# Optimization experiments

Measured on AMD Instinct MI355X. Metric: run time of the kernel, lower is better.

Reference implementation:

```python
import jax, jax.numpy as jnp
import numpy as np

B, S, E, H, D = 1, 2048, 1024, 16, 64
LAM_INIT = 0.8  # \u03bbinit from init_kwargs
LN_EPS = 1e-5


def setup_inputs() -> dict:
    key = jax.random.key(0)
    ks = jax.random.split(key, 6)
    w = 0.02  # weight init scale
    return {
        "X": jax.random.normal(ks[0], (B, S, E), dtype=jnp.float32),
        "Wq": jax.random.normal(ks[1], (H, E, 2 * D), dtype=jnp.float32) * w,
        "bq": jnp.zeros((H, 2 * D), dtype=jnp.float32),
        "Wk": jax.random.normal(ks[2], (H, E, 2 * D), dtype=jnp.float32) * w,
        "bk": jnp.zeros((H, 2 * D), dtype=jnp.float32),
        "Wv": jax.random.normal(ks[3], (H, E, D), dtype=jnp.float32) * w,
        "bv": jnp.zeros((H, D), dtype=jnp.float32),
        "Wo": jax.random.normal(ks[4], (H * D, E), dtype=jnp.float32) * w,
        "bo": jnp.zeros((E,), dtype=jnp.float32),
        "gamma": jnp.ones((E,), dtype=jnp.float32),
        "beta": jnp.zeros((E,), dtype=jnp.float32),
        "lam": jnp.float32(0.5),
    }


def reference(X, Wq, bq, Wk, bk, Wv, bv, Wo, bo, gamma, beta, lam):
    # Batched over heads: Q,K -> [B,H,S,2D], V -> [B,H,S,D]
    Q = jnp.einsum("bse,hec->bhsc", X, Wq) + bq[None, :, None, :]
    K = jnp.einsum("bse,hec->bhsc", X, Wk) + bk[None, :, None, :]
    V = jnp.einsum("bse,hed->bhsd", X, Wv) + bv[None, :, None, :]
    d = Wv.shape[-1]
    Q1, Q2 = Q[..., :d], Q[..., d:]
    K1, K2 = K[..., :d], K[..., d:]
    s = 1.0 / jnp.sqrt(jnp.float32(d))
    A1 = jnp.einsum("bhqd,bhkd->bhqk", Q1, K1) * s
    A2 = jnp.einsum("bhqd,bhkd->bhqk", Q2, K2) * s
    P = jax.nn.softmax(A1, axis=-1) - lam * jax.nn.softmax(A2, axis=-1)
    O = jnp.einsum("bhqk,bhkd->bhqd", P, V)  # [B,H,S,D]
    Ocat = jnp.transpose(O, (0, 2, 1, 3)).reshape(O.shape[0], O.shape[2], -1)  # [B,S,H*D]
    Y = Ocat @ Wo + bo
    mu = jnp.mean(Y, axis=-1, keepdims=True)
    var = jnp.var(Y, axis=-1, keepdims=True)
    Yn = (Y - mu) * jax.lax.rsqrt(var + LN_EPS) * gamma + beta
    return Yn * (1.0 - LAM_INIT)
```

## Files before the change

### kernel.cpp

```cpp
#include <hip/hip_runtime.h>

#define S_LEN 2048
#define EDIM  1024
#define HEADS 16
#define DHEAD 64

typedef __attribute__((ext_vector_type(8))) short bf16x8;
typedef __attribute__((ext_vector_type(4))) short short4v;
typedef __attribute__((ext_vector_type(4))) float f32x4;

__device__ inline unsigned short f2bf(float f) {
    unsigned int u = __float_as_uint(f);
    unsigned int r = (u + 0x7FFFu + ((u >> 16) & 1u)) >> 16;
    return (unsigned short)r;
}
__device__ inline float bf2f(unsigned short b) {
    return __uint_as_float(((unsigned int)b) << 16);
}
__device__ inline void load_lds16(const void* g, void* l) {
    __builtin_amdgcn_global_load_lds(
        (const __attribute__((address_space(1))) unsigned int*)g,
        (__attribute__((address_space(3))) unsigned int*)l, 16, 0, 0);
}

__global__ void k_convert_x(const float* __restrict__ x, short* __restrict__ xb, int n4) {
    int i = blockIdx.x * blockDim.x + threadIdx.x;
    if (i >= n4) return;
    f32x4 v = ((const f32x4*)x)[i];
    short4v o;
    o[0] = (short)f2bf(v[0]); o[1] = (short)f2bf(v[1]);
    o[2] = (short)f2bf(v[2]); o[3] = (short)f2bf(v[3]);
    ((short4v*)xb)[i] = o;
}

__global__ void k_transpose_cvt(const float* __restrict__ in, short* __restrict__ out, int R, int C) {
    __shared__ float tile[32][33];
    const int b = blockIdx.z;
    in  += (size_t)b * R * C;
    out += (size_t)b * R * C;
    const int c0 = blockIdx.x * 32, r0 = blockIdx.y * 32;
    #pragma unroll
    for (int yy = 0; yy < 4; ++yy) {
        int r = r0 + threadIdx.y + yy * 8, c = c0 + threadIdx.x;
        tile[threadIdx.y + yy * 8][threadIdx.x] = (r < R && c < C) ? in[(size_t)r * C + c] : 0.f;
    }
    __syncthreads();
    #pragma unroll
    for (int yy = 0; yy < 4; ++yy) {
        int c = c0 + threadIdx.y + yy * 8, r = r0 + threadIdx.x;
        if (c < C && r < R) out[(size_t)c * R + r] = (short)f2bf(tile[threadIdx.x][threadIdx.y + yy * 8]);
    }
}

template<int BM, int BN, int WR, int WC>
__device__ inline void gemm_core(const char* Ag, int ldaB, const char* Bg, int ldbB,
                                 int K, char* sA, char* sB, f32x4* acc) {
    constexpr int NW = WR * WC;
    constexpr int FM = BM / (WR * 16), FN = BN / (WC * 16);
    constexpr int CA = (BM * 128) / (1024 * NW);
    constexpr int CB = (BN * 128) / (1024 * NW);
    const int lane = threadIdx.x & 63, wave = threadIdx.x >> 6;
    const int rl = lane & 15, g = lane >> 4;
    const int wrow = (wave / WC) * (BM / WR);
    const int wcol = (wave % WC) * (BN / WC);
    const int lr = lane >> 3;
    const int lc = ((lane & 7) ^ lr) << 4;

    for (int t = 0; t < K / 64; ++t) {
        __syncthreads();
        #pragma unroll
        for (int i = 0; i < CA; ++i) {
            const int c = i * NW + wave;
            load_lds16(Ag + (size_t)(c * 8 + lr) * ldaB + t * 128 + lc, sA + c * 1024);
        }
        #pragma unroll
        for (int i = 0; i < CB; ++i) {
            const int c = i * NW + wave;
            load_lds16(Bg + (size_t)(c * 8 + lr) * ldbB + t * 128 + lc, sB + c * 1024);
        }
        __syncthreads();
        #pragma unroll
        for (int kk = 0; kk < 2; ++kk) {
            bf16x8 af[FM], bf[FN];
            #pragma unroll
            for (int f = 0; f < FM; ++f) {
                const int r = wrow + f * 16 + rl;
                af[f] = *(const bf16x8*)(sA + r * 128 + (((kk * 4 + g) ^ (r & 7)) << 4));
            }
            #pragma unroll
            for (int j = 0; j < FN; ++j) {
                const int r = wcol + j * 16 + rl;
                bf[j] = *(const bf16x8*)(sB + r * 128 + (((kk * 4 + g) ^ (r & 7)) << 4));
            }
            #pragma unroll
            for (int f = 0; f < FM; ++f)
                #pragma unroll
                for (int j = 0; j < FN; ++j)
                    acc[f * FN + j] = __builtin_amdgcn_mfma_f32_16x16x32_bf16(af[f], bf[j], acc[f * FN + j], 0, 0, 0);
        }
    }
}

__global__ __launch_bounds__(512) void k_gemm_qkv(
        const short* __restrict__ Xb,
        const short* __restrict__ WqT, const short* __restrict__ WkT, const short* __restrict__ WvT,
        const float* __restrict__ bq, const float* __restrict__ bk, const float* __restrict__ bv,
        short* __restrict__ Qh, short* __restrict__ Kh, short* __restrict__ Vt) {
    __shared__ __align__(16) char sA[16384], sB[16384];
    int id = blockIdx.x;
    id = (id & 7) * 80 + (id >> 3);
    const int mbase = (id % 16) * 128;
    const int y = id / 16;

    const short* Bt; const float* bias; int nbase; int which;
    if (y < 16)      { which = 0; Bt = WqT; bias = bq; nbase = y * 128; }
    else if (y < 32) { which = 1; Bt = WkT; bias = bk; nbase = (y - 16) * 128; }
    else             { which = 2; Bt = WvT; bias = bv; nbase = (y - 32) * 128; }

    f32x4 acc[8];
    #pragma unroll
    for (int i = 0; i < 8; ++i) acc[i] = (f32x4){0.f, 0.f, 0.f, 0.f};

    gemm_core<128, 128, 2, 4>((const char*)Xb + (size_t)mbase * 2048, 2048,
                              (const char*)Bt + (size_t)nbase * 2048, 2048,
                              EDIM, sA, sB, acc);

    const int lane = threadIdx.x & 63, wave = threadIdx.x >> 6;
    const int wr = (wave >> 2) * 64, wc = (wave & 3) * 32;
    const int rl = lane & 15, g = lane >> 4;
    const float qscale = 0.125f * 1.44269504088896f;
    #pragma unroll
    for (int i = 0; i < 4; ++i)
        #pragma unroll
        for (int j = 0; j < 2; ++j)
            #pragma unroll
            for (int jj = 0; jj < 4; ++jj) {
                int s = mbase + wr + i * 16 + g * 4 + jj;
                int n = nbase + wc + j * 16 + rl;
                float v = acc[i * 2 + j][jj] + bias[n];
                if (which == 0) v *= qscale;
                short b16 = (short)f2bf(v);
                if (which == 0)      Qh[((size_t)(n >> 7) * S_LEN + s) * 128 + (n & 127)] = b16;
                else if (which == 1) Kh[((size_t)(n >> 7) * S_LEN + s) * 128 + (n & 127)] = b16;
                else                 Vt[(size_t)n * S_LEN + s] = b16;
            }
}

__global__ __launch_bounds__(512, 4) void k_attn(
        const short* __restrict__ Qh, const short* __restrict__ Kh,
        const short* __restrict__ Vt, const float* __restrict__ lam_p,
        short* __restrict__ Ocat) {
    __shared__ __align__(16) char smem[49152];

    const int lane = threadIdx.x & 63, wave = threadIdx.x >> 6;
    const int rl = lane & 15, g = lane >> 4;
    const int qw = wave & 3, kvg = wave >> 2;
    const int h = blockIdx.y;
    const int qbase = blockIdx.x * 64 + qw * 16;
    const int kx = rl & 7;
    const int swz = (rl & 7) << 4;
    const float MFIX = 6.0f;

    char* Kg0 = smem + kvg * 16384;
    char* Pw  = smem + 32768 + wave * 2048;

    const char* Kgb = (const char*)(Kh + (size_t)h * S_LEN * 128);
    const char* Vgb = (const char*)(Vt + (size_t)h * DHEAD * S_LEN);
    const short* Qp = Qh + (size_t)h * S_LEN * 128;

    const int kc0 = qw * 2, kc1 = qw * 2 + 1;
    const int kofs0 = (lane >> 4) * 256 + (((lane & 15) ^ (lane >> 4)) << 4);
    const int kofs1 = (lane >> 4) * 256 + (((lane & 15) ^ ((lane >> 4) + 4)) << 4);

    auto STAGE = [&](int b, int it) {
        const size_t kv0 = (size_t)(kvg * 1024 + it * 32);
        char* kb = Kg0 + b * 8192;
        load_lds16(Kgb + (kv0 + (size_t)kc0 * 4) * 256 + kofs0, kb + kc0 * 1024);
        load_lds16(Kgb + (kv0 + (size_t)kc1 * 4) * 256 + kofs1, kb + kc1 * 1024);
    };

    STAGE(0, 0);

    bf16x8 qf[2][2];
    #pragma unroll
    for (int p = 0; p < 2; ++p)
        #pragma unroll
        for (int kc = 0; kc < 2; ++kc)
            qf[p][kc] = *(const bf16x8*)&Qp[(size_t)(qbase + rl) * 128 + p * 64 + kc * 32 + g * 8];

    bf16x8 ones;
    #pragma unroll
    for (int i = 0; i < 8; ++i) ones[i] = (short)0x3F80;

    f32x4 acc[2][4], accL[2];
    #pragma unroll
    for (int p = 0; p < 2; ++p) {
        #pragma unroll
        for (int t = 0; t < 4; ++t) acc[p][t] = (f32x4){0.f, 0.f, 0.f, 0.f};
        accL[p] = (f32x4){0.f, 0.f, 0.f, 0.f};
    }

    __syncthreads();

    const int NIT = 1024 / 32;
    for (int it = 0; it < NIT; ++it) {
        const int cur = it & 1;
        if (it + 1 < NIT) STAGE(cur ^ 1, it + 1);
        const char* kb = Kg0 + cur * 8192;
        const size_t kv0 = (size_t)(kvg * 1024 + it * 32);

        bf16x8 vf[4];
        #pragma unroll
        for (int t = 0; t < 4; ++t)
            vf[t] = *(const bf16x8*)(Vgb + (size_t)(t * 16 + rl) * 4096 + (kv0 + g * 8) * 2);

        #pragma unroll
        for (int p = 0; p < 2; ++p) {
            f32x4 sc[2];
            #pragma unroll
            for (int t = 0; t < 2; ++t) {
                f32x4 z = (f32x4){0.f, 0.f, 0.f, 0.f};
                #pragma unroll
                for (int kc = 0; kc < 2; ++kc) {
                    bf16x8 kf = *(const bf16x8*)(kb + t * 4096 + rl * 256 + (((p * 8 + kc * 4 + g) ^ kx) << 4));
                    z = __builtin_amdgcn_mfma_f32_16x16x32_bf16(kf, qf[p][kc], z, 0, 0, 0);
                }
                sc[t] = z;
            }

            #pragma unroll
            for (int t = 0; t < 2; ++t) {
                #pragma unroll
                for (int jjp = 0; jjp < 4; jjp += 2) {
                    float e0 = exp2f(sc[t][jjp]     - MFIX);
                    float e1 = exp2f(sc[t][jjp + 1] - MFIX);
                    unsigned u;
                    asm("v_cvt_pk_bf16_f32 %0, %1, %2" : "=v"(u) : "v"(e0), "v"(e1));
                    *(unsigned*)(Pw + rl * 128 + ((p * 64 + (t * 16 + g * 4 + jjp) * 2) ^ swz)) = u;
                }
            }

            bf16x8 pa = *(const bf16x8*)(Pw + rl * 128 + ((p * 64 + g * 16) ^ swz));
            accL[p] = __builtin_amdgcn_mfma_f32_16x16x32_bf16(pa, ones, accL[p], 0, 0, 0);
            #pragma unroll
            for (int t = 0; t < 4; ++t)
                acc[p][t] = __builtin_amdgcn_mfma_f32_16x16x32_bf16(pa, vf[t], acc[p][t], 0, 0, 0);
        }
        __syncthreads();
    }

    {
        unsigned short* Xw = (unsigned short*)(smem + wave * 4096);
        float* ML = (float*)(smem + 32768);
        #pragma unroll
        for (int p = 0; p < 2; ++p) {
            #pragma unroll
            for (int t = 0; t < 4; ++t)
                #pragma unroll
                for (int jj = 0; jj < 4; ++jj)
                    Xw[p * 1024 + (g * 4 + jj) * 64 + t * 16 + rl] = f2bf(acc[p][t][jj]);
            if (rl == 0) {
                #pragma unroll
                for (int jj = 0; jj < 4; ++jj)
                    ML[(wave * 2 + p) * 16 + g * 4 + jj] = accL[p][jj];
            }
        }
    }
    __syncthreads();

    {
        const int q = threadIdx.x >> 3, d0 = (threadIdx.x & 7) * 8;
        const int q15 = q & 15, wa = q >> 4, wb = (q >> 4) + 4;
        const float* ML = (const float*)(smem + 32768);
        const float lam = lam_p[0];
        float res[2][8];
        float invL[2];
        #pragma unroll
        for (int p = 0; p < 2; ++p) {
            float la = ML[(wa * 2 + p) * 16 + q15];
            float lb = ML[(wb * 2 + p) * 16 + q15];
            invL[p] = 1.0f / (la + lb);
            const unsigned short* xa = (const unsigned short*)(smem + wa * 4096 + p * 2048 + q15 * 128 + d0 * 2);
            const unsigned short* xb = (const unsigned short*)(smem + wb * 4096 + p * 2048 + q15 * 128 + d0 * 2);
            #pragma unroll
            for (int k = 0; k < 8; ++k)
                res[p][k] = bf2f(xa[k]) + bf2f(xb[k]);
        }
        bf16x8 ov;
        #pragma unroll
        for (int k = 0; k < 8; ++k)
            ov[k] = (short)f2bf(res[0][k] * invL[0] - lam * res[1][k] * invL[1]);
        *(bf16x8*)&Ocat[(size_t)(blockIdx.x * 64 + q) * 1024 + h * 64 + d0] = ov;
    }
}

__global__ __launch_bounds__(512) void k_gemm_out(
        const short* __restrict__ Ocat, const short* __restrict__ WoT,
        const float* __restrict__ bo, float* __restrict__ Yws) {
    __shared__ __align__(16) char sA[8192], sB[16384];
    int id = blockIdx.x;
    id = (id & 7) * 32 + (id >> 3);
    const int mbase = (id % 32) * 64;
    const int nbase = (id / 32) * 128;

    f32x4 acc[4];
    #pragma unroll
    for (int i = 0; i < 4; ++i) acc[i] = (f32x4){0.f, 0.f, 0.f, 0.f};

    gemm_core<64, 128, 2, 4>((const char*)Ocat + (size_t)mbase * 2048, 2048,
                             (const char*)WoT + (size_t)nbase * 2048, 2048,
                             1024, sA, sB, acc);

    const int lane = threadIdx.x & 63, wave = threadIdx.x >> 6;
    const int wr = (wave >> 2) * 32, wc = (wave & 3) * 32;
    const int rl = lane & 15, g = lane >> 4;
    #pragma unroll
    for (int f = 0; f < 2; ++f)
        #pragma unroll
        for (int j = 0; j < 2; ++j)
            #pragma unroll
            for (int jj = 0; jj < 4; ++jj) {
                int s = mbase + wr + f * 16 + g * 4 + jj;
                int e = nbase + wc + j * 16 + rl;
                Yws[(size_t)s * 1024 + e] = acc[f * 2 + j][jj] + bo[e];
            }
}

__global__ __launch_bounds__(256) void k_ln(
        const float* __restrict__ Yws, const float* __restrict__ gamma,
        const float* __restrict__ beta, float* __restrict__ out) {
    const int s = blockIdx.x;
    const int tid = threadIdx.x;
    f32x4 y = ((const f32x4*)(Yws + (size_t)s * 1024))[tid];
    float sum = y[0] + y[1] + y[2] + y[3];
    float sq  = y[0]*y[0] + y[1]*y[1] + y[2]*y[2] + y[3]*y[3];
    #pragma unroll
    for (int off = 1; off < 64; off <<= 1) {
        sum += __shfl_xor(sum, off, 64);
        sq  += __shfl_xor(sq,  off, 64);
    }
    __shared__ float ls[2][4];
    const int wave = tid >> 6, lane = tid & 63;
    if (lane == 0) { ls[0][wave] = sum; ls[1][wave] = sq; }
    __syncthreads();
    sum = ls[0][0] + ls[0][1] + ls[0][2] + ls[0][3];
    sq  = ls[1][0] + ls[1][1] + ls[1][2] + ls[1][3];
    const float mu = sum * (1.f / 1024.f);
    const float var = sq * (1.f / 1024.f) - mu * mu;
    const float rstd = rsqrtf(var + 1e-5f);
    f32x4 gg = ((const f32x4*)gamma)[tid];
    f32x4 bb = ((const f32x4*)beta)[tid];
    f32x4 o;
    #pragma unroll
    for (int k = 0; k < 4; ++k)
        o[k] = ((y[k] - mu) * rstd * gg[k] + bb[k]) * 0.2f;
    ((f32x4*)(out + (size_t)s * 1024))[tid] = o;
}

extern "C" void kernel_launch(void* const* d_in, const int* in_sizes, int n_in,
                              void* d_out, int out_size, void* d_ws, size_t ws_size,
                              hipStream_t stream) {
    const float* X     = (const float*)d_in[0];
    const float* Wq    = (const float*)d_in[1];
    const float* bq    = (const float*)d_in[2];
    const float* Wk    = (const float*)d_in[3];
    const float* bk    = (const float*)d_in[4];
    const float* Wv    = (const float*)d_in[5];
    const float* bv    = (const float*)d_in[6];
    const float* Wo    = (const float*)d_in[7];
    const float* bo    = (const float*)d_in[8];
    const float* gamma = (const float*)d_in[9];
    const float* beta  = (const float*)d_in[10];
    const float* lam   = (const float*)d_in[11];
    float* out = (float*)d_out;

    char* ws = (char*)d_ws;
    const size_t MB = 1u << 20;
    short* Xb  = (short*)(ws + 0);
    short* WqT = (short*)(ws + 4 * MB);
    short* WkT = (short*)(ws + 8 * MB);
    short* WvT = (short*)(ws + 12 * MB);
    short* WoT = (short*)(ws + 14 * MB);
    short* Qh  = (short*)(ws + 16 * MB);
    short* Kh  = (short*)(ws + 24 * MB);
    short* Vt  = (short*)(ws + 32 * MB);
    short* Oc  = (short*)(ws + 36 * MB);
    float* Yws = (float*)(ws + 0);

    k_convert_x<<<dim3(2048), dim3(256), 0, stream>>>(X, Xb, (S_LEN * EDIM) / 4);
    k_transpose_cvt<<<dim3(4, 32, 16), dim3(32, 8), 0, stream>>>(Wq, WqT, 1024, 128);
    k_transpose_cvt<<<dim3(4, 32, 16), dim3(32, 8), 0, stream>>>(Wk, WkT, 1024, 128);
    k_transpose_cvt<<<dim3(2, 32, 16), dim3(32, 8), 0, stream>>>(Wv, WvT, 1024, 64);
    k_transpose_cvt<<<dim3(32, 32, 1), dim3(32, 8), 0, stream>>>(Wo, WoT, 1024, 1024);
    k_gemm_qkv<<<dim3(640), dim3(512), 0, stream>>>(Xb, WqT, WkT, WvT, bq, bk, bv, Qh, Kh, Vt);
    k_attn<<<dim3(32, 16), dim3(512), 0, stream>>>(Qh, Kh, Vt, lam, Oc);
    k_gemm_out<<<dim3(256), dim3(512), 0, stream>>>(Oc, WoT, bo, Yws);
    k_ln<<<dim3(2048), dim3(256), 0, stream>>>(Yws, gamma, beta, out);
}
```

Before: 161.4 us.

## Split attention waves across the two score halves and halve the query tile

Each wave now handles one 16-query group and one of the two differential-attention halves (p), rather than 16 queries for both halves. Blocks cover 32 queries instead of 64, so twice as many blocks launch, LDS use drops to 40 KB and the launch-bounds target rises to 8 blocks. The aim is fewer registers per wave and higher occupancy and parallelism. The cost is that each K tile is loaded into LDS for half as many queries, doubling K and V global traffic per query, and the final reduction writes narrower 4-element stores.

```diff
diff --git a/kernel.cpp b/kernel.cpp
--- a/kernel.cpp
+++ b/kernel.cpp
@@ -146,34 +146,34 @@
             }
 }
 
-__global__ __launch_bounds__(512, 4) void k_attn(
+__global__ __launch_bounds__(512, 8) void k_attn(
         const short* __restrict__ Qh, const short* __restrict__ Kh,
         const short* __restrict__ Vt, const float* __restrict__ lam_p,
         short* __restrict__ Ocat) {
-    __shared__ __align__(16) char smem[49152];
+    __shared__ __align__(16) char smem[40960];
 
     const int lane = threadIdx.x & 63, wave = threadIdx.x >> 6;
     const int rl = lane & 15, g = lane >> 4;
-    const int qw = wave & 3, kvg = wave >> 2;
+    const int qw = wave & 1, p = (wave >> 1) & 1, kvh = wave >> 2;
     const int h = blockIdx.y;
-    const int qbase = blockIdx.x * 64 + qw * 16;
-    const int kx = rl & 7;
+    const int qbase = blockIdx.x * 32 + qw * 16;
     const int swz = (rl & 7) << 4;
     const float MFIX = 6.0f;
 
-    char* Kg0 = smem + kvg * 16384;
-    char* Pw  = smem + 32768 + wave * 2048;
+    char* Kg0 = smem + kvh * 16384;
+    char* Pw  = smem + 32768 + (qw + kvh * 2) * 2048;
 
     const char* Kgb = (const char*)(Kh + (size_t)h * S_LEN * 128);
     const char* Vgb = (const char*)(Vt + (size_t)h * DHEAD * S_LEN);
     const short* Qp = Qh + (size_t)h * S_LEN * 128;
 
-    const int kc0 = qw * 2, kc1 = qw * 2 + 1;
+    const int gi = wave & 3;
+    const int kc0 = gi * 2, kc1 = gi * 2 + 1;
     const int kofs0 = (lane >> 4) * 256 + (((lane & 15) ^ (lane >> 4)) << 4);
     const int kofs1 = (lane >> 4) * 256 + (((lane & 15) ^ ((lane >> 4) + 4)) << 4);
 
     auto STAGE = [&](int b, int it) {
-        const size_t kv0 = (size_t)(kvg * 1024 + it * 32);
+        const size_t kv0 = (size_t)(kvh * 1024 + it * 32);
         char* kb = Kg0 + b * 8192;
         load_lds16(Kgb + (kv0 + (size_t)kc0 * 4) * 256 + kofs0, kb + kc0 * 1024);
         load_lds16(Kgb + (kv0 + (size_t)kc1 * 4) * 256 + kofs1, kb + kc1 * 1024);
@@ -181,24 +181,19 @@
 
     STAGE(0, 0);
 
-    bf16x8 qf[2][2];
-    #pragma unroll
-    for (int p = 0; p < 2; ++p)
-        #pragma unroll
-        for (int kc = 0; kc < 2; ++kc)
-            qf[p][kc] = *(const bf16x8*)&Qp[(size_t)(qbase + rl) * 128 + p * 64 + kc * 32 + g * 8];
+    bf16x8 qf[2];
+    #pragma unroll
+    for (int kc = 0; kc < 2; ++kc)
+        qf[kc] = *(const bf16x8*)&Qp[(size_t)(qbase + rl) * 128 + p * 64 + kc * 32 + g * 8];
 
     bf16x8 ones;
     #pragma unroll
     for (int i = 0; i < 8; ++i) ones[i] = (short)0x3F80;
 
-    f32x4 acc[2][4], accL[2];
-    #pragma unroll
-    for (int p = 0; p < 2; ++p) {
-        #pragma unroll
-        for (int t = 0; t < 4; ++t) acc[p][t] = (f32x4){0.f, 0.f, 0.f, 0.f};
-        accL[p] = (f32x4){0.f, 0.f, 0.f, 0.f};
-    }
+    f32x4 acc[4], accL;
+    #pragma unroll
+    for (int t = 0; t < 4; ++t) acc[t] = (f32x4){0.f, 0.f, 0.f, 0.f};
+    accL = (f32x4){0.f, 0.f, 0.f, 0.f};
 
     __syncthreads();
 
@@ -207,90 +202,88 @@
         const int cur = it & 1;
         if (it + 1 < NIT) STAGE(cur ^ 1, it + 1);
         const char* kb = Kg0 + cur * 8192;
-        const size_t kv0 = (size_t)(kvg * 1024 + it * 32);
+        const size_t kv0 = (size_t)(kvh * 1024 + it * 32);
 
         bf16x8 vf[4];
         #pragma unroll
         for (int t = 0; t < 4; ++t)
             vf[t] = *(const bf16x8*)(Vgb + (size_t)(t * 16 + rl) * 4096 + (kv0 + g * 8) * 2);
 
-        #pragma unroll
-        for (int p = 0; p < 2; ++p) {
-            f32x4 sc[2];
-            #pragma unroll
-            for (int t = 0; t < 2; ++t) {
-                f32x4 z = (f32x4){0.f, 0.f, 0.f, 0.f};
-                #pragma unroll
-                for (int kc = 0; kc < 2; ++kc) {
-                    bf16x8 kf = *(const bf16x8*)(kb + t * 4096 + rl * 256 + (((p * 8 + kc * 4 + g) ^ kx) << 4));
-                    z = __builtin_amdgcn_mfma_f32_16x16x32_bf16(kf, qf[p][kc], z, 0, 0, 0);
-                }
-                sc[t] = z;
-            }
-
-            #pragma unroll
-            for (int t = 0; t < 2; ++t) {
-                #pragma unroll
-                for (int jjp = 0; jjp < 4; jjp += 2) {
-                    float e0 = exp2f(sc[t][jjp]     - MFIX);
-                    float e1 = exp2f(sc[t][jjp + 1] - MFIX);
-                    unsigned u;
-                    asm("v_cvt_pk_bf16_f32 %0, %1, %2" : "=v"(u) : "v"(e0), "v"(e1));
-                    *(unsigned*)(Pw + rl * 128 + ((p * 64 + (t * 16 + g * 4 + jjp) * 2) ^ swz)) = u;
-                }
-            }
-
-            bf16x8 pa = *(const bf16x8*)(Pw + rl * 128 + ((p * 64 + g * 16) ^ swz));
-            accL[p] = __builtin_amdgcn_mfma_f32_16x16x32_bf16(pa, ones, accL[p], 0, 0, 0);
-            #pragma unroll
-            for (int t = 0; t < 4; ++t)
-                acc[p][t] = __builtin_amdgcn_mfma_f32_16x16x32_bf16(pa, vf[t], acc[p][t], 0, 0, 0);
-        }
+        f32x4 sc[2];
+        #pragma unroll
+        for (int t = 0; t < 2; ++t) {
+            f32x4 z = (f32x4){0.f, 0.f, 0.f, 0.f};
+            #pragma unroll
+            for (int kc = 0; kc < 2; ++kc) {
+                bf16x8 kf = *(const bf16x8*)(kb + (t * 16 + rl) * 256 +
+                                ((p * 128 + kc * 64 + g * 16) ^ swz));
+                z = __builtin_amdgcn_mfma_f32_16x16x32_bf16(kf, qf[kc], z, 0, 0, 0);
+            }
+            sc[t] = z;
+        }
+
+        #pragma unroll
+        for (int t = 0; t < 2; ++t) {
+            #pragma unroll
+            for (int jjp = 0; jjp < 4; jjp += 2) {
+                float e0 = exp2f(sc[t][jjp]     - MFIX);
+                float e1 = exp2f(sc[t][jjp + 1] - MFIX);
+                unsigned u;
+                asm("v_cvt_pk_bf16_f32 %0, %1, %2" : "=v"(u) : "v"(e0), "v"(e1));
+                *(unsigned*)(Pw + rl * 128 + ((p * 64 + (t * 16 + g * 4 + jjp) * 2) ^ swz)) = u;
+            }
+        }
+
+        bf16x8 pa = *(const bf16x8*)(Pw + rl * 128 + ((p * 64 + g * 16) ^ swz));
+        accL = __builtin_amdgcn_mfma_f32_16x16x32_bf16(pa, ones, accL, 0, 0, 0);
+        #pragma unroll
+        for (int t = 0; t < 4; ++t)
+            acc[t] = __builtin_amdgcn_mfma_f32_16x16x32_bf16(pa, vf[t], acc[t], 0, 0, 0);
+
         __syncthreads();
     }
 
+    __syncthreads();
     {
-        unsigned short* Xw = (unsigned short*)(smem + wave * 4096);
-        float* ML = (float*)(smem + 32768);
-        #pragma unroll
-        for (int p = 0; p < 2; ++p) {
-            #pragma unroll
-            for (int t = 0; t < 4; ++t)
-                #pragma unroll
-                for (int jj = 0; jj < 4; ++jj)
-                    Xw[p * 1024 + (g * 4 + jj) * 64 + t * 16 + rl] = f2bf(acc[p][t][jj]);
-            if (rl == 0) {
-                #pragma unroll
-                for (int jj = 0; jj < 4; ++jj)
-                    ML[(wave * 2 + p) * 16 + g * 4 + jj] = accL[p][jj];
-            }
+        unsigned short* Xw = (unsigned short*)(smem + wave * 2048);
+        float* ML = (float*)(smem + 16384);
+        #pragma unroll
+        for (int t = 0; t < 4; ++t)
+            #pragma unroll
+            for (int jj = 0; jj < 4; ++jj)
+                Xw[(g * 4 + jj) * 64 + t * 16 + rl] = f2bf(acc[t][jj]);
+        if (rl == 0) {
+            #pragma unroll
+            for (int jj = 0; jj < 4; ++jj)
+                ML[wave * 16 + g * 4 + jj] = accL[jj];
         }
     }
     __syncthreads();
 
     {
-        const int q = threadIdx.x >> 3, d0 = (threadIdx.x & 7) * 8;
-        const int q15 = q & 15, wa = q >> 4, wb = (q >> 4) + 4;
-        const float* ML = (const float*)(smem + 32768);
+        const int q = threadIdx.x >> 4, d0 = (threadIdx.x & 15) * 4;
+        const int q15 = q & 15, qws = q >> 4;
+        const float* ML = (const float*)(smem + 16384);
         const float lam = lam_p[0];
-        float res[2][8];
+        float res[2][4];
         float invL[2];
         #pragma unroll
-        for (int p = 0; p < 2; ++p) {
-            float la = ML[(wa * 2 + p) * 16 + q15];
-            float lb = ML[(wb * 2 + p) * 16 + q15];
-            invL[p] = 1.0f / (la + lb);
-            const unsigned short* xa = (const unsigned short*)(smem + wa * 4096 + p * 2048 + q15 * 128 + d0 * 2);
-            const unsigned short* xb = (const unsigned short*)(smem + wb * 4096 + p * 2048 + q15 * 128 + d0 * 2);
-            #pragma unroll
-            for (int k = 0; k < 8; ++k)
-                res[p][k] = bf2f(xa[k]) + bf2f(xb[k]);
-        }
-        bf16x8 ov;
-        #pragma unroll
-        for (int k = 0; k < 8; ++k)
+        for (int pp = 0; pp < 2; ++pp) {
+            const int wa = qws + pp * 2, wb = wa + 4;
+            float la = ML[wa * 16 + q15];
+            float lb = ML[wb * 16 + q15];
+            invL[pp] = 1.0f / (la + lb);
+            const unsigned short* xa = (const unsigned short*)(smem + wa * 2048) + q15 * 64 + d0;
+            const unsigned short* xb = (const unsigned short*)(smem + wb * 2048) + q15 * 64 + d0;
+            #pragma unroll
+            for (int k = 0; k < 4; ++k)
+                res[pp][k] = bf2f(xa[k]) + bf2f(xb[k]);
+        }
+        short4v ov;
+        #pragma unroll
+        for (int k = 0; k < 4; ++k)
             ov[k] = (short)f2bf(res[0][k] * invL[0] - lam * res[1][k] * invL[1]);
-        *(bf16x8*)&Ocat[(size_t)(blockIdx.x * 64 + q) * 1024 + h * 64 + d0] = ov;
+        *(short4v*)&Ocat[(size_t)(blockIdx.x * 32 + q) * 1024 + h * 64 + d0] = ov;
     }
 }
 
@@ -393,7 +386,7 @@
     k_transpose_cvt<<<dim3(2, 32, 16), dim3(32, 8), 0, stream>>>(Wv, WvT, 1024, 64);
     k_transpose_cvt<<<dim3(32, 32, 1), dim3(32, 8), 0, stream>>>(Wo, WoT, 1024, 1024);
     k_gemm_qkv<<<dim3(640), dim3(512), 0, stream>>>(Xb, WqT, WkT, WvT, bq, bk, bv, Qh, Kh, Vt);
-    k_attn<<<dim3(32, 16), dim3(512), 0, stream>>>(Qh, Kh, Vt, lam, Oc);
+    k_attn<<<dim3(64, 16), dim3(512), 0, stream>>>(Qh, Kh, Vt, lam, Oc);
     k_gemm_out<<<dim3(256), dim3(512), 0, stream>>>(Oc, WoT, bo, Yws);
     k_ln<<<dim3(2048), dim3(256), 0, stream>>>(Yws, gamma, beta, out);
 }
```

New measurement: 220.6 us. 36.7% more time.
